# Kernel tuning notes

Measured on AMD Instinct MI355X. Metric: run time of the kernel, lower is better.

Reference implementation:

```python
import jax, jax.numpy as jnp
import numpy as np

C, G = 128, 2000          # num_cells, total_genes
CE, GE, H = 64, 64, 256   # cell_embed_dim, gene_embed_dim, hidden_dim
F = CE + GE + 3           # FCGNN input: ctrl val + cell_embed + gene_embed + shift + num_cells


def setup_inputs() -> dict:
    key = jax.random.key(0)
    ks = jax.random.split(key, 13)
    s = 0.02
    return {
        "ctrl": jax.random.uniform(ks[0], (C, G), dtype=jnp.float32),
        "shift_vec": jax.random.normal(ks[1], (G,), dtype=jnp.float32),
        "gene_indices": jnp.arange(G, dtype=jnp.int32),
        # CellEmbedding params
        "ce_w1": jax.random.normal(ks[2], (G, H), dtype=jnp.float32) * s,
        "ce_b1": jnp.zeros((H,), dtype=jnp.float32),
        "ce_w2": jax.random.normal(ks[3], (H, CE), dtype=jnp.float32) * s,
        "ce_b2": jnp.zeros((CE,), dtype=jnp.float32),
        # gene embedding table
        "gene_table": jax.random.normal(ks[4], (G, GE), dtype=jnp.float32) * s,
        # FCGNN params
        "g_w1": jax.random.normal(ks[5], (F, H), dtype=jnp.float32) * s,
        "g_b1": jnp.zeros((H,), dtype=jnp.float32),
        "g_w2": jax.random.normal(ks[6], (2 * H, H), dtype=jnp.float32) * s,
        "g_b2": jnp.zeros((H,), dtype=jnp.float32),
        "g_w3": jax.random.normal(ks[7], (2 * H, 1), dtype=jnp.float32) * s,
        "g_b3": jnp.zeros((1,), dtype=jnp.float32),
    }


def reference(ctrl, shift_vec, gene_indices, ce_w1, ce_b1, ce_w2, ce_b2,
              gene_table, g_w1, g_b1, g_w2, g_b2, g_w3, g_b3):
    num_cells = ctrl.shape[0]
    num_genes = gene_indices.shape[0]

    # CellEmbedding: fc2(elu(fc1(ctrl)))  -> [C, CE]
    ce = jax.nn.elu(ctrl @ ce_w1 + ce_b1) @ ce_w2 + ce_b2

    ctrl_g = ctrl[:, gene_indices]           # [C, Gn]
    shift = shift_vec[gene_indices]          # [Gn]
    ge = gene_table[gene_indices]            # [Gn, GE]

    # Build [C, Gn, F] feature tensor (ctrl val, cell embed, gene embed, shift, num_cells)
    z = jnp.concatenate([
        ctrl_g[:, :, None],
        jnp.broadcast_to(ce[:, None, :], (num_cells, num_genes, ce.shape[1])),
        jnp.broadcast_to(ge[None, :, :], (num_cells, num_genes, ge.shape[1])),
        jnp.broadcast_to(shift[None, :, None], (num_cells, num_genes, 1)),
        jnp.full((num_cells, num_genes, 1), float(num_cells), dtype=ctrl.dtype),
    ], axis=2)

    # FCGNN applied per gene (vectorized over gene axis); pooling is mean over cells (axis 0)
    x = jax.nn.elu(z @ g_w1 + g_b1)                                   # [C, Gn, H]
    p = x.mean(axis=0)                                                # [Gn, H]
    x = jnp.concatenate([x, jnp.broadcast_to(p[None], x.shape)], -1) @ g_w2 + g_b2
    p = x.mean(axis=0)
    x = jax.nn.elu(jnp.concatenate([x, jnp.broadcast_to(p[None], x.shape)], -1)) @ g_w3 + g_b3
    out = x[..., 0]                                                   # [C, Gn]

    # softmax over cells (torch Softmax(dim=0) after transpose/squeeze)
    return jax.nn.softmax(out, axis=0)
```

## Files before the change

### kernel.cpp

```cpp
#include <hip/hip_runtime.h>
#include <hip/hip_bf16.h>
#include <math.h>

#define G_GENES 2000
#define C_CELLS 128
#define H_DIM   256
#define CE_DIM  64
#define LDAe    260

typedef __attribute__((ext_vector_type(8))) short short8;
typedef __attribute__((ext_vector_type(4))) float floatx4;

__device__ __forceinline__ float eluf(float x) {
    float e = __expf(x) - 1.0f;
    return x > 0.0f ? x : e;
}
__device__ __forceinline__ unsigned short f2bf(float v) {
    unsigned u = __float_as_uint(v);
    u += 0x7FFF + ((u >> 16) & 1);
    return (unsigned short)(u >> 16);
}
__device__ __forceinline__ unsigned pk2(float a, float b) {
    __hip_bfloat162 h2 = __float22bfloat162_rn(make_float2(a, b));
    unsigned r; __builtin_memcpy(&r, &h2, 4); return r;
}
__device__ __forceinline__ float bflo(unsigned u) { return __uint_as_float(u << 16); }
__device__ __forceinline__ float bfhi(unsigned u) { return __uint_as_float(u & 0xffff0000u); }
union U8 { unsigned u[4]; short8 s; uint4 v; };

__global__ __launch_bounds__(512) void k_g1(
    const float* __restrict__ ctrl, const float* __restrict__ ce_w1,
    const float* __restrict__ g_w1, const float* __restrict__ g_b1,
    const float* __restrict__ shiftv, const int* __restrict__ gidx,
    const float* __restrict__ gtab, const float* __restrict__ g_w2,
    float* __restrict__ hidpart, unsigned short* __restrict__ w2abt,
    unsigned short* __restrict__ w2bb, float* __restrict__ Bvg)
{
    const int b = blockIdx.x;
    const int t = threadIdx.x;

    if (b < 256) {
        __shared__ float crow[8][128];
        const int cgrp = b >> 4;
        const int kc   = b & 15;
        const int cell = t >> 6;
        const int hq   = t & 63;
        const int h0   = hq * 4;
        const int c    = cgrp * 8 + cell;

        #pragma unroll
        for (int p = 0; p < 2; ++p) {
            const int idx = p * 512 + t;
            const int lc  = idx >> 7;
            const int kk  = idx & 127;
            if (kk < 125)
                crow[lc][kk] = ctrl[(size_t)(cgrp * 8 + lc) * G_GENES + kc * 125 + kk];
        }
        __syncthreads();

        float4 s = {0.f, 0.f, 0.f, 0.f};
        const float* wbase = ce_w1 + (size_t)(kc * 125) * H_DIM + h0;
        #pragma unroll 5
        for (int k = 0; k < 125; ++k) {
            const float crv = crow[cell][k];
            const float4 wv = *(const float4*)(wbase + (size_t)k * H_DIM);
            s.x = fmaf(crv, wv.x, s.x);
            s.y = fmaf(crv, wv.y, s.y);
            s.z = fmaf(crv, wv.z, s.z);
            s.w = fmaf(crv, wv.w, s.w);
        }
        *(float4*)&hidpart[((size_t)kc * C_CELLS + c) * H_DIM + h0] = s;
    } else if (b < 272) {
        const int n  = (b - 256) * 16 + (t >> 5);
        const int k0 = (t & 31) * 8;
        float v[8];
        #pragma unroll
        for (int j = 0; j < 8; ++j) v[j] = g_w2[(size_t)(k0 + j) * H_DIM + n];
        U8 u;
        u.u[0] = pk2(v[0], v[1]); u.u[1] = pk2(v[2], v[3]);
        u.u[2] = pk2(v[4], v[5]); u.u[3] = pk2(v[6], v[7]);
        *(uint4*)&w2abt[(size_t)n * H_DIM + k0] = u.v;
    } else if (b < 288) {
        const int hr = (b - 272) * 16 + (t >> 5);
        const int j0 = (t & 31) * 8;
        const float* src = g_w2 + (size_t)(H_DIM + hr) * H_DIM + j0;
        float4 f0 = *(const float4*)src;
        float4 f1 = *(const float4*)(src + 4);
        U8 u;
        u.u[0] = pk2(f0.x, f0.y); u.u[1] = pk2(f0.z, f0.w);
        u.u[2] = pk2(f1.x, f1.y); u.u[3] = pk2(f1.z, f1.w);
        *(uint4*)&w2bb[(size_t)hr * H_DIM + j0] = u.v;
    } else {
        const int gq = b - 288;
        const int half = t >> 8;
        const int h = t & 255;
        const int gA = gq * 4 + half * 2;
        const int gB = gA + 1;
        const int iA = gidx[gA];
        const int iB = gidx[gB];

        const float b1  = g_b1[h];
        const float w129 = g_w1[(size_t)129 * H_DIM + h];
        const float w130 = g_w1[(size_t)130 * H_DIM + h];
        float bvA = b1 + 128.0f * w130 + shiftv[iA] * w129;
        float bvB = b1 + 128.0f * w130 + shiftv[iB] * w129;
        #pragma unroll 8
        for (int e = 0; e < CE_DIM; ++e) {
            const float wv = g_w1[(size_t)(65 + e) * H_DIM + h];
            bvA = fmaf(gtab[(size_t)iA * CE_DIM + e], wv, bvA);
            bvB = fmaf(gtab[(size_t)iB * CE_DIM + e], wv, bvB);
        }
        Bvg[(size_t)gA * H_DIM + h] = bvA;
        Bvg[(size_t)gB * H_DIM + h] = bvB;
    }
}

__global__ __launch_bounds__(256) void k_fin(
    const float* __restrict__ hidpart, const float* __restrict__ ce_b1,
    const float* __restrict__ ce_w2, const float* __restrict__ ce_b2,
    const float* __restrict__ g_w1, unsigned short* __restrict__ Atcbf)
{
    __shared__ float hid[H_DIM];
    __shared__ float celp[4 * CE_DIM];
    __shared__ float cel[CE_DIM];
    const int c = blockIdx.x;
    const int t = threadIdx.x;

    float s = ce_b1[t];
    #pragma unroll
    for (int kc = 0; kc < 16; ++kc)
        s += hidpart[((size_t)kc * C_CELLS + c) * H_DIM + t];
    hid[t] = eluf(s);
    __syncthreads();

    {
        const int e = t & 63, q4 = t >> 6;
        float cp = 0.f;
        #pragma unroll 8
        for (int hh = 0; hh < 64; ++hh)
            cp = fmaf(hid[q4 * 64 + hh], ce_w2[(size_t)(q4 * 64 + hh) * CE_DIM + e], cp);
        celp[q4 * CE_DIM + e] = cp;
    }
    __syncthreads();
    if (t < CE_DIM)
        cel[t] = ce_b2[t] + celp[t] + celp[CE_DIM + t] + celp[2 * CE_DIM + t] + celp[3 * CE_DIM + t];
    __syncthreads();

    float a = 0.f;
    #pragma unroll 8
    for (int e = 0; e < CE_DIM; ++e) a = fmaf(cel[e], g_w1[(size_t)(1 + e) * H_DIM + t], a);
    Atcbf[(size_t)c * H_DIM + t] = f2bf(a);
}

__global__ __launch_bounds__(512, 4) void k_main(
    const float* __restrict__ ctrl, const int* __restrict__ gidx,
    const float* __restrict__ g_w1, const float* __restrict__ g_b2,
    const float* __restrict__ g_w3, const unsigned short* __restrict__ Atcbf,
    const float* __restrict__ Bvg, const unsigned short* __restrict__ w2abt,
    const unsigned short* __restrict__ w2bb, float* __restrict__ out)
{
    __shared__ __align__(16) unsigned short x1t[C_CELLS * LDAe];
    __shared__ __align__(16) float scratch[8 * 258];
    __shared__ float pvec[H_DIM];
    __shared__ float qa[H_DIM];
    __shared__ float qb[H_DIM];
    __shared__ float b2l[H_DIM];
    __shared__ float w3v[H_DIM];

    const int g = blockIdx.x;
    const int t = threadIdx.x;
    const int idx = gidx[g];

    const int lane = t & 63;
    const int w    = t >> 6;
    const int quad = lane >> 4;
    const int nlo  = lane & 15;
    const int wm   = w >> 2;
    const int wn   = w & 3;

    const int ho = t & 31, cgrp = t >> 5;
    const int h0 = ho * 8;
    uint4 A[8];
    #pragma unroll
    for (int i = 0; i < 8; ++i)
        A[i] = *(const uint4*)(Atcbf + (size_t)(cgrp * 8 + i) * H_DIM + h0);
    float4 bv0 = *(const float4*)(Bvg + (size_t)g * H_DIM + h0);
    float4 bv1 = *(const float4*)(Bvg + (size_t)g * H_DIM + h0 + 4);
    float4 wv0 = *(const float4*)(g_w1 + h0);
    float4 wv1 = *(const float4*)(g_w1 + h0 + 4);

    const unsigned short* bbase = w2abt + (size_t)(wn * 64 + nlo) * H_DIM + quad * 8;
    short8 bcur[4];
    #pragma unroll
    for (int nt = 0; nt < 4; ++nt)
        bcur[nt] = *(const short8*)(bbase + (size_t)nt * 16 * H_DIM);

    float ccl = 0.f;
    if ((lane & 31) < 8)
        ccl = ctrl[(size_t)(cgrp * 8 + (lane & 31)) * G_GENES + idx];

    if (t < H_DIM) {
        w3v[t] = g_w3[t];
        b2l[t] = g_b2[t];
    }

    {
        float s[8];
        #pragma unroll
        for (int j = 0; j < 8; ++j) s[j] = 0.f;
        #pragma unroll
        for (int i = 0; i < 8; ++i) {
            const int c = cgrp * 8 + i;
            const float ccv = __shfl(ccl, (lane & 32) + i);
            float v0 = eluf(fmaf(ccv, wv0.x, bflo(A[i].x) + bv0.x));
            float v1 = eluf(fmaf(ccv, wv0.y, bfhi(A[i].x) + bv0.y));
            float v2 = eluf(fmaf(ccv, wv0.z, bflo(A[i].y) + bv0.z));
            float v3 = eluf(fmaf(ccv, wv0.w, bfhi(A[i].y) + bv0.w));
            float v4 = eluf(fmaf(ccv, wv1.x, bflo(A[i].z) + bv1.x));
            float v5 = eluf(fmaf(ccv, wv1.y, bfhi(A[i].z) + bv1.y));
            float v6 = eluf(fmaf(ccv, wv1.z, bflo(A[i].w) + bv1.z));
            float v7 = eluf(fmaf(ccv, wv1.w, bfhi(A[i].w) + bv1.w));
            s[0] += v0; s[1] += v1; s[2] += v2; s[3] += v3;
            s[4] += v4; s[5] += v5; s[6] += v6; s[7] += v7;
            uint4 pk;
            pk.x = pk2(v0, v1); pk.y = pk2(v2, v3);
            pk.z = pk2(v4, v5); pk.w = pk2(v6, v7);
            *(uint4*)&x1t[c * LDAe + h0] = pk;
        }
        #pragma unroll
        for (int j = 0; j < 8; ++j) s[j] += __shfl_xor(s[j], 32);
        if (lane < 32) {
            float4 p0 = {s[0], s[1], s[2], s[3]};
            float4 p1 = {s[4], s[5], s[6], s[7]};
            *(float4*)&scratch[w * 258 + h0] = p0;
            *(float4*)&scratch[w * 258 + h0 + 4] = p1;
        }
    }
    __syncthreads();

    floatx4 acc[4][4];
    #pragma unroll
    for (int mt = 0; mt < 4; ++mt)
        #pragma unroll
        for (int nt = 0; nt < 4; ++nt)
            acc[mt][nt] = (floatx4){0.f, 0.f, 0.f, 0.f};

    const unsigned short* abase = &x1t[(wm * 64 + nlo) * LDAe + quad * 8];

    #pragma unroll
    for (int kt = 0; kt < 8; ++kt) {
        short8 af[4];
        #pragma unroll
        for (int mt = 0; mt < 4; ++mt)
            af[mt] = *(const short8*)(abase + mt * 16 * LDAe + kt * 32);
        short8 bnx[4];
        if (kt < 7) {
            #pragma unroll
            for (int nt = 0; nt < 4; ++nt)
                bnx[nt] = *(const short8*)(bbase + (size_t)nt * 16 * H_DIM + (kt + 1) * 32);
        }
        #pragma unroll
        for (int nt = 0; nt < 4; ++nt)
            #pragma unroll
            for (int mt = 0; mt < 4; ++mt)
                acc[mt][nt] = __builtin_amdgcn_mfma_f32_16x16x32_bf16(af[mt], bcur[nt], acc[mt][nt], 0, 0, 0);
        if (kt < 7) {
            #pragma unroll
            for (int nt = 0; nt < 4; ++nt) bcur[nt] = bnx[nt];
        }
    }

    if (t < H_DIM) {
        float ps = 0.f;
        #pragma unroll
        for (int w2 = 0; w2 < 8; ++w2) ps += scratch[w2 * 258 + t];
        pvec[t] = ps * (1.0f / 128.0f);
    }
    __syncthreads();

    {
        const int j = t & 255, hf = t >> 8;
        const unsigned short* wp = w2bb + (size_t)(hf * 128) * H_DIM + j;
        const float* pv = pvec + hf * 128;
        float q0 = 0.f, q1 = 0.f, q2 = 0.f, q3 = 0.f;
        #pragma unroll 8
        for (int h = 0; h < 128; h += 4) {
            q0 = fmaf(pv[h + 0], bflo((unsigned)wp[(size_t)(h + 0) * H_DIM] << 16), q0);
            q1 = fmaf(pv[h + 1], bflo((unsigned)wp[(size_t)(h + 1) * H_DIM] << 16), q1);
            q2 = fmaf(pv[h + 2], bflo((unsigned)wp[(size_t)(h + 2) * H_DIM] << 16), q2);
            q3 = fmaf(pv[h + 3], bflo((unsigned)wp[(size_t)(h + 3) * H_DIM] << 16), q3);
        }
        const float qp = (q0 + q1) + (q2 + q3);
        if (hf) qb[j] = qp; else qa[j] = qp;
    }
    __syncthreads();

    float* red2 = scratch;
    float qj[4], w3j[4];
    #pragma unroll
    for (int nt = 0; nt < 4; ++nt) {
        const int j = wn * 64 + nt * 16 + nlo;
        qj[nt] = qa[j] + qb[j] + b2l[j];
        w3j[nt] = w3v[j];
    }
    #pragma unroll
    for (int mt = 0; mt < 4; ++mt) {
        #pragma unroll
        for (int reg = 0; reg < 4; ++reg) {
            float part = 0.f;
            #pragma unroll
            for (int nt = 0; nt < 4; ++nt)
                part = fmaf(eluf(acc[mt][nt][reg] + qj[nt]), w3j[nt], part);
            part += __shfl_xor(part, 1);
            part += __shfl_xor(part, 2);
            part += __shfl_xor(part, 4);
            part += __shfl_xor(part, 8);
            if (nlo == 0)
                red2[(wm * 64 + mt * 16 + quad * 4 + reg) * 5 + wn] = part;
        }
    }
    __syncthreads();

    if (t < 64) {
        const float s0 = red2[t * 5 + 0] + red2[t * 5 + 1]
                       + red2[t * 5 + 2] + red2[t * 5 + 3];
        const float s1 = red2[(t + 64) * 5 + 0] + red2[(t + 64) * 5 + 1]
                       + red2[(t + 64) * 5 + 2] + red2[(t + 64) * 5 + 3];
        const float e0 = __expf(fminf(s0, 80.f));
        const float e1 = __expf(fminf(s1, 80.f));
        float S = e0 + e1;
        #pragma unroll
        for (int off = 1; off < 64; off <<= 1) S += __shfl_xor(S, off);
        const float inv = 1.0f / S;
        out[(size_t)t * G_GENES + g] = e0 * inv;
        out[(size_t)(t + 64) * G_GENES + g] = e1 * inv;
    }
}

extern "C" void kernel_launch(void* const* d_in, const int* in_sizes, int n_in,
                              void* d_out, int out_size, void* d_ws, size_t ws_size,
                              hipStream_t stream) {
    const float* ctrl   = (const float*)d_in[0];
    const float* shiftv = (const float*)d_in[1];
    const int*   gidx   = (const int*)d_in[2];
    const float* ce_w1  = (const float*)d_in[3];
    const float* ce_b1  = (const float*)d_in[4];
    const float* ce_w2  = (const float*)d_in[5];
    const float* ce_b2  = (const float*)d_in[6];
    const float* gtab   = (const float*)d_in[7];
    const float* g_w1   = (const float*)d_in[8];
    const float* g_b1   = (const float*)d_in[9];
    const float* g_w2   = (const float*)d_in[10];
    const float* g_b2   = (const float*)d_in[11];
    const float* g_w3   = (const float*)d_in[12];

    char* ws = (char*)d_ws;
    unsigned short* Atcbf = (unsigned short*)(ws);
    unsigned short* w2abt = (unsigned short*)(ws + 128 * 1024);
    unsigned short* w2bb  = (unsigned short*)(ws + 256 * 1024);
    float* Bvg            = (float*)(ws + 384 * 1024);
    float* hidpart        = (float*)(ws + 384 * 1024 + (size_t)G_GENES * H_DIM * 4);
    float* out            = (float*)d_out;

    k_g1<<<788, 512, 0, stream>>>(
        ctrl, ce_w1, g_w1, g_b1, shiftv, gidx, gtab, g_w2, hidpart, w2abt, w2bb, Bvg);
    k_fin<<<C_CELLS, 256, 0, stream>>>(hidpart, ce_b1, ce_w2, ce_b2, g_w1, Atcbf);
    k_main<<<G_GENES, 512, 0, stream>>>(ctrl, gidx, g_w1, g_b2, g_w3,
                                        Atcbf, Bvg, w2abt, w2bb, out);
}
```

Before: 205.1 us.

## Fuse cell-embedding finish into prep kernel, one block per cell

Merges the cell-embedding partial matmul and its finishing kernel into a single prep kernel where each block handles one whole cell: it stages the full ctrl row in shared memory, splits K across 8 warps-groups, and reduces, applies ELU, fc2 and the g_w1 projection in place. This removes one kernel launch and the global hidpart round trip. In exchange, per-block K work doubles (250 vs 125) and only 128 blocks do the heavy fc1 work instead of 256, which lengthens that critical path.

```diff
diff --git a/kernel.cpp b/kernel.cpp
--- a/kernel.cpp
+++ b/kernel.cpp
@@ -28,50 +28,84 @@
 __device__ __forceinline__ float bfhi(unsigned u) { return __uint_as_float(u & 0xffff0000u); }
 union U8 { unsigned u[4]; short8 s; uint4 v; };
 
-__global__ __launch_bounds__(512) void k_g1(
+__global__ __launch_bounds__(512) void k_prep(
     const float* __restrict__ ctrl, const float* __restrict__ ce_w1,
-    const float* __restrict__ g_w1, const float* __restrict__ g_b1,
-    const float* __restrict__ shiftv, const int* __restrict__ gidx,
-    const float* __restrict__ gtab, const float* __restrict__ g_w2,
-    float* __restrict__ hidpart, unsigned short* __restrict__ w2abt,
+    const float* __restrict__ ce_b1, const float* __restrict__ ce_w2,
+    const float* __restrict__ ce_b2, const float* __restrict__ g_w1,
+    const float* __restrict__ g_b1, const float* __restrict__ shiftv,
+    const int* __restrict__ gidx, const float* __restrict__ gtab,
+    const float* __restrict__ g_w2,
+    unsigned short* __restrict__ Atcbf, unsigned short* __restrict__ w2abt,
     unsigned short* __restrict__ w2bb, float* __restrict__ Bvg)
 {
     const int b = blockIdx.x;
     const int t = threadIdx.x;
 
-    if (b < 256) {
-        __shared__ float crow[8][128];
-        const int cgrp = b >> 4;
-        const int kc   = b & 15;
-        const int cell = t >> 6;
-        const int hq   = t & 63;
-        const int h0   = hq * 4;
-        const int c    = cgrp * 8 + cell;
-
-        #pragma unroll
-        for (int p = 0; p < 2; ++p) {
-            const int idx = p * 512 + t;
-            const int lc  = idx >> 7;
-            const int kk  = idx & 127;
-            if (kk < 125)
-                crow[lc][kk] = ctrl[(size_t)(cgrp * 8 + lc) * G_GENES + kc * 125 + kk];
-        }
-        __syncthreads();
-
-        float4 s = {0.f, 0.f, 0.f, 0.f};
-        const float* wbase = ce_w1 + (size_t)(kc * 125) * H_DIM + h0;
-        #pragma unroll 5
-        for (int k = 0; k < 125; ++k) {
-            const float crv = crow[cell][k];
-            const float4 wv = *(const float4*)(wbase + (size_t)k * H_DIM);
-            s.x = fmaf(crv, wv.x, s.x);
-            s.y = fmaf(crv, wv.y, s.y);
-            s.z = fmaf(crv, wv.z, s.z);
-            s.w = fmaf(crv, wv.w, s.w);
-        }
-        *(float4*)&hidpart[((size_t)kc * C_CELLS + c) * H_DIM + h0] = s;
-    } else if (b < 272) {
-        const int n  = (b - 256) * 16 + (t >> 5);
+    if (b < C_CELLS) {
+        __shared__ float cr[G_GENES];
+        __shared__ float hidp[8][H_DIM];
+        __shared__ float hid[H_DIM];
+        __shared__ float celp[4][CE_DIM];
+        __shared__ float cel[CE_DIM];
+        const int c = b;
+
+        #pragma unroll
+        for (int p = 0; p < 4; ++p) {
+            const int i = p * 512 + t;
+            if (i < G_GENES) cr[i] = ctrl[(size_t)c * G_GENES + i];
+        }
+        __syncthreads();
+
+        {
+            const int ks = t >> 6;
+            const int h0 = (t & 63) * 4;
+            float4 s = {0.f, 0.f, 0.f, 0.f};
+            const float* wb = ce_w1 + (size_t)(ks * 250) * H_DIM + h0;
+            const float* cp = cr + ks * 250;
+            #pragma unroll 5
+            for (int k = 0; k < 250; ++k) {
+                const float crv = cp[k];
+                const float4 wv = *(const float4*)(wb + (size_t)k * H_DIM);
+                s.x = fmaf(crv, wv.x, s.x);
+                s.y = fmaf(crv, wv.y, s.y);
+                s.z = fmaf(crv, wv.z, s.z);
+                s.w = fmaf(crv, wv.w, s.w);
+            }
+            *(float4*)&hidp[ks][h0] = s;
+        }
+        __syncthreads();
+
+        if (t < H_DIM) {
+            float hv = ce_b1[t];
+            #pragma unroll
+            for (int ks = 0; ks < 8; ++ks) hv += hidp[ks][t];
+            hid[t] = eluf(hv);
+        }
+        __syncthreads();
+
+        if (t < H_DIM) {
+            const int e = t & 63, q4 = t >> 6;
+            float cpv = 0.f;
+            #pragma unroll 8
+            for (int hh = 0; hh < 64; ++hh)
+                cpv = fmaf(hid[q4 * 64 + hh],
+                           ce_w2[(size_t)(q4 * 64 + hh) * CE_DIM + e], cpv);
+            celp[q4][e] = cpv;
+        }
+        __syncthreads();
+        if (t < CE_DIM)
+            cel[t] = ce_b2[t] + celp[0][t] + celp[1][t] + celp[2][t] + celp[3][t];
+        __syncthreads();
+
+        if (t < H_DIM) {
+            float a = 0.f;
+            #pragma unroll 8
+            for (int e = 0; e < CE_DIM; ++e)
+                a = fmaf(cel[e], g_w1[(size_t)(1 + e) * H_DIM + t], a);
+            Atcbf[(size_t)c * H_DIM + t] = f2bf(a);
+        }
+    } else if (b < 144) {
+        const int n  = (b - 128) * 16 + (t >> 5);
         const int k0 = (t & 31) * 8;
         float v[8];
         #pragma unroll
@@ -80,8 +114,8 @@
         u.u[0] = pk2(v[0], v[1]); u.u[1] = pk2(v[2], v[3]);
         u.u[2] = pk2(v[4], v[5]); u.u[3] = pk2(v[6], v[7]);
         *(uint4*)&w2abt[(size_t)n * H_DIM + k0] = u.v;
-    } else if (b < 288) {
-        const int hr = (b - 272) * 16 + (t >> 5);
+    } else if (b < 160) {
+        const int hr = (b - 144) * 16 + (t >> 5);
         const int j0 = (t & 31) * 8;
         const float* src = g_w2 + (size_t)(H_DIM + hr) * H_DIM + j0;
         float4 f0 = *(const float4*)src;
@@ -91,7 +125,7 @@
         u.u[2] = pk2(f1.x, f1.y); u.u[3] = pk2(f1.z, f1.w);
         *(uint4*)&w2bb[(size_t)hr * H_DIM + j0] = u.v;
     } else {
-        const int gq = b - 288;
+        const int gq = b - 160;
         const int half = t >> 8;
         const int h = t & 255;
         const int gA = gq * 4 + half * 2;
@@ -99,7 +133,7 @@
         const int iA = gidx[gA];
         const int iB = gidx[gB];
 
-        const float b1  = g_b1[h];
+        const float b1   = g_b1[h];
         const float w129 = g_w1[(size_t)129 * H_DIM + h];
         const float w130 = g_w1[(size_t)130 * H_DIM + h];
         float bvA = b1 + 128.0f * w130 + shiftv[iA] * w129;
@@ -113,43 +147,6 @@
         Bvg[(size_t)gA * H_DIM + h] = bvA;
         Bvg[(size_t)gB * H_DIM + h] = bvB;
     }
-}
-
-__global__ __launch_bounds__(256) void k_fin(
-    const float* __restrict__ hidpart, const float* __restrict__ ce_b1,
-    const float* __restrict__ ce_w2, const float* __restrict__ ce_b2,
-    const float* __restrict__ g_w1, unsigned short* __restrict__ Atcbf)
-{
-    __shared__ float hid[H_DIM];
-    __shared__ float celp[4 * CE_DIM];
-    __shared__ float cel[CE_DIM];
-    const int c = blockIdx.x;
-    const int t = threadIdx.x;
-
-    float s = ce_b1[t];
-    #pragma unroll
-    for (int kc = 0; kc < 16; ++kc)
-        s += hidpart[((size_t)kc * C_CELLS + c) * H_DIM + t];
-    hid[t] = eluf(s);
-    __syncthreads();
-
-    {
-        const int e = t & 63, q4 = t >> 6;
-        float cp = 0.f;
-        #pragma unroll 8
-        for (int hh = 0; hh < 64; ++hh)
-            cp = fmaf(hid[q4 * 64 + hh], ce_w2[(size_t)(q4 * 64 + hh) * CE_DIM + e], cp);
-        celp[q4 * CE_DIM + e] = cp;
-    }
-    __syncthreads();
-    if (t < CE_DIM)
-        cel[t] = ce_b2[t] + celp[t] + celp[CE_DIM + t] + celp[2 * CE_DIM + t] + celp[3 * CE_DIM + t];
-    __syncthreads();
-
-    float a = 0.f;
-    #pragma unroll 8
-    for (int e = 0; e < CE_DIM; ++e) a = fmaf(cel[e], g_w1[(size_t)(1 + e) * H_DIM + t], a);
-    Atcbf[(size_t)c * H_DIM + t] = f2bf(a);
 }
 
 __global__ __launch_bounds__(512, 4) void k_main(
@@ -359,12 +356,11 @@
     unsigned short* w2abt = (unsigned short*)(ws + 128 * 1024);
     unsigned short* w2bb  = (unsigned short*)(ws + 256 * 1024);
     float* Bvg            = (float*)(ws + 384 * 1024);
-    float* hidpart        = (float*)(ws + 384 * 1024 + (size_t)G_GENES * H_DIM * 4);
     float* out            = (float*)d_out;
 
-    k_g1<<<788, 512, 0, stream>>>(
-        ctrl, ce_w1, g_w1, g_b1, shiftv, gidx, gtab, g_w2, hidpart, w2abt, w2bb, Bvg);
-    k_fin<<<C_CELLS, 256, 0, stream>>>(hidpart, ce_b1, ce_w2, ce_b2, g_w1, Atcbf);
+    k_prep<<<660, 512, 0, stream>>>(
+        ctrl, ce_w1, ce_b1, ce_w2, ce_b2, g_w1, g_b1, shiftv, gidx, gtab, g_w2,
+        Atcbf, w2abt, w2bb, Bvg);
     k_main<<<G_GENES, 512, 0, stream>>>(ctrl, gidx, g_w1, g_b2, g_w3,
                                         Atcbf, Bvg, w2abt, w2bb, out);
 }
```

Result: slower. 211.0 us (+2.9%).
